# Performance work log

Hardware: AMD Instinct MI355X
Metric: run time of the kernel (lower is better)

Reference implementation:

```python
import jax, jax.numpy as jnp
import numpy as np

ALPHA = 0.65   # module default
KSIZE = 7      # kernel_size
T = 1.0        # forward arg t default


def setup_inputs() -> dict:
    key = jax.random.key(0)
    k1, k2 = jax.random.split(key)
    x = jax.random.normal(k1, (4, 32, 128, 128), dtype=jnp.float32)
    dil_metric = jax.random.normal(k2, (32, 2, 2), dtype=jnp.float32)
    return {"x": x, "dil_metric": dil_metric}


def _kernel(dil_metric):
    # y grid: [k,k,2] integer offsets centered at floor(k/2) (matches get_y)
    c = jnp.arange(KSIZE, dtype=jnp.float32) - (KSIZE // 2)
    yi, yj = jnp.meshgrid(c, c, indexing="ij")
    y = jnp.stack([yi, yj], axis=-1)                       # [k,k,2]
    Dy = jnp.einsum("cab,ijb->cija", dil_metric, y)        # [C,k,k,2]
    sumsq = jnp.sum(Dy * Dy, axis=-1)                      # [C,k,k] = norm^2
    p = 2.0 * ALPHA / (2.0 * ALPHA - 1.0)
    const = T * (2.0 * ALPHA - 1.0) / (2.0 * ALPHA * T) ** p
    # const * norm**p written as const * (norm^2)^(p/2) (same math, smooth at 0)
    return const * jnp.power(sumsq, p / 2.0)               # [C,k,k]


def reference(x, dil_metric):
    # dilation: -inf_convolution_2d(-x, kernel)
    kern = _kernel(dil_metric)                             # [C,k,k]
    H, W = x.shape[2], x.shape[3]
    pad = (KSIZE - 1) // 2                                 # k odd -> symmetric pad
    xp = jnp.pad(-x, ((0, 0), (0, 0), (pad, pad), (pad, pad)))  # zero pad like torch
    out = None
    # fixed small k*k loop over window offsets; min-plus conv without im2col blowup
    for i in range(KSIZE):
        for j in range(KSIZE):
            v = xp[:, :, i:i + H, j:j + W] + kern[:, i, j][None, :, None, None]
            out = v if out is None else jnp.minimum(out, v)
    return -out
```

## Files before the change

kernel.cpp:

```cpp
#include <hip/hip_runtime.h>
#include <math.h>

#define KS   7
#define PAD  3
#define TH   8
#define W128 128
#define HALO_H (TH + KS - 1)
#define HALO_W (W128 + KS - 1)

__global__ __launch_bounds__(256) void dilation_r2_kernel(
    const float* __restrict__ x,
    const float* __restrict__ dm,
    float* __restrict__ out)
{
    __shared__ float ksm[KS * KS];
    __shared__ float sx[HALO_H][HALO_W];

    const int tid  = threadIdx.x;
    const int tile = blockIdx.x;
    const int c    = blockIdx.y;
    const int n    = blockIdx.z;
    const int h0   = tile * TH;

    if (tid < KS * KS) {
        const int i = tid / KS, j = tid % KS;
        const float yi = (float)(i - PAD);
        const float yj = (float)(j - PAD);
        const float m00 = dm[c * 4 + 0], m01 = dm[c * 4 + 1];
        const float m10 = dm[c * 4 + 2], m11 = dm[c * 4 + 3];
        const float d0 = m00 * yi + m01 * yj;
        const float d1 = m10 * yi + m11 * yj;
        const float s  = d0 * d0 + d1 * d1;
        const float pc = (float)(0.3 / pow(1.3, 13.0 / 3.0));
        ksm[tid] = pc * powf(s, (float)(13.0 / 6.0));
    }

    const float* xc = x + ((size_t)(n * 32 + c)) * (W128 * W128);
    for (int idx = tid; idx < HALO_H * HALO_W; idx += 256) {
        const int r  = idx / HALO_W;
        const int cc = idx - r * HALO_W;
        const int gh = h0 + r - PAD;
        const int gw = cc - PAD;
        float v = 0.0f;
        if (gh >= 0 && gh < W128 && gw >= 0 && gw < W128)
            v = xc[gh * W128 + gw];
        sx[r][cc] = v;
    }
    __syncthreads();

    const int w  = tid & (W128 - 1);
    const int hq = (tid >> 7) * 4;
    float acc0 = -INFINITY, acc1 = -INFINITY, acc2 = -INFINITY, acc3 = -INFINITY;

    #pragma unroll
    for (int j = 0; j < KS; ++j) {
        float col[TH / 2 + KS - 1];
        #pragma unroll
        for (int r = 0; r < TH / 2 + KS - 1; ++r)
            col[r] = sx[hq + r][w + j];
        #pragma unroll
        for (int i = 0; i < KS; ++i) {
            const float k = ksm[i * KS + j];
            acc0 = fmaxf(acc0, col[i + 0] - k);
            acc1 = fmaxf(acc1, col[i + 1] - k);
            acc2 = fmaxf(acc2, col[i + 2] - k);
            acc3 = fmaxf(acc3, col[i + 3] - k);
        }
    }

    float* oc = out + ((size_t)(n * 32 + c)) * (W128 * W128) + (h0 + hq) * W128 + w;
    oc[0 * W128] = acc0;
    oc[1 * W128] = acc1;
    oc[2 * W128] = acc2;
    oc[3 * W128] = acc3;
}

extern "C" void kernel_launch(void* const* d_in, const int* in_sizes, int n_in,
                              void* d_out, int out_size, void* d_ws, size_t ws_size,
                              hipStream_t stream) {
    const float* x  = (const float*)d_in[0];
    const float* dm = (const float*)d_in[1];
    float* out = (float*)d_out;

    dim3 grid(W128 / TH, 32, 4);
    dim3 block(256);
    dilation_r2_kernel<<<grid, block, 0, stream>>>(x, dm, out);
}
```

Measured before the change: 13.41 us.

## Use taller tiles with 4x4 register blocking and vectorized loads/stores

Tile height grows from 8 to 32 rows, so the halo overhead per block shrinks, and the grid drops from 2048 blocks to 512. Global loads and stores now use float4, and shared memory rows are padded to a stride of 136. Each thread computes a 4x4 output patch from rows held in registers, with the negated kernel kept in registers and pre-folded into the min-plus taps. The risks are fewer blocks to hide latency on a large GPU and higher register pressure.

```diff
diff --git a/kernel.cpp b/kernel.cpp
--- a/kernel.cpp
+++ b/kernel.cpp
@@ -1,78 +1,112 @@
 #include <hip/hip_runtime.h>
 #include <math.h>
 
-#define KS   7
-#define PAD  3
-#define TH   8
-#define W128 128
-#define HALO_H (TH + KS - 1)
-#define HALO_W (W128 + KS - 1)
+typedef float f4 __attribute__((ext_vector_type(4)));
 
-__global__ __launch_bounds__(256) void dilation_r2_kernel(
+#define KS     7
+#define W      128
+#define TILE_H 32
+#define HALO_H (TILE_H + KS - 1)
+#define STR    136
+#define CHK    (STR / 4)
+#define NCHK   (HALO_H * CHK)
+
+__global__ __launch_bounds__(256) void dil_kernel(
     const float* __restrict__ x,
     const float* __restrict__ dm,
     float* __restrict__ out)
 {
-    __shared__ float ksm[KS * KS];
-    __shared__ float sx[HALO_H][HALO_W];
+    __shared__ __align__(16) float ksm[52];
+    __shared__ __align__(16) float sx[HALO_H * STR];
 
-    const int tid  = threadIdx.x;
-    const int tile = blockIdx.x;
-    const int c    = blockIdx.y;
-    const int n    = blockIdx.z;
-    const int h0   = tile * TH;
+    const int tid = threadIdx.x;
+    const int c   = blockIdx.y;
+    const int n   = blockIdx.z;
+    const int h0  = blockIdx.x * TILE_H;
 
-    if (tid < KS * KS) {
-        const int i = tid / KS, j = tid % KS;
-        const float yi = (float)(i - PAD);
-        const float yj = (float)(j - PAD);
-        const float m00 = dm[c * 4 + 0], m01 = dm[c * 4 + 1];
-        const float m10 = dm[c * 4 + 2], m11 = dm[c * 4 + 3];
-        const float d0 = m00 * yi + m01 * yj;
-        const float d1 = m10 * yi + m11 * yj;
-        const float s  = d0 * d0 + d1 * d1;
-        const float pc = (float)(0.3 / pow(1.3, 13.0 / 3.0));
-        ksm[tid] = pc * powf(s, (float)(13.0 / 6.0));
+    if (tid < 52) {
+        float v = -1e30f;
+        if (tid < 49) {
+            const int i = tid / KS, j = tid % KS;
+            const float yi = (float)(i - 3), yj = (float)(j - 3);
+            const float m00 = dm[c*4+0], m01 = dm[c*4+1];
+            const float m10 = dm[c*4+2], m11 = dm[c*4+3];
+            const float d0 = m00*yi + m01*yj;
+            const float d1 = m10*yi + m11*yj;
+            const float s  = d0*d0 + d1*d1;
+            const float pc = (float)(0.3 / pow(1.3, 13.0/3.0));
+            v = -(pc * powf(s, (float)(13.0/6.0)));
+        }
+        ksm[tid] = v;
     }
 
-    const float* xc = x + ((size_t)(n * 32 + c)) * (W128 * W128);
-    for (int idx = tid; idx < HALO_H * HALO_W; idx += 256) {
-        const int r  = idx / HALO_W;
-        const int cc = idx - r * HALO_W;
-        const int gh = h0 + r - PAD;
-        const int gw = cc - PAD;
-        float v = 0.0f;
-        if (gh >= 0 && gh < W128 && gw >= 0 && gw < W128)
-            v = xc[gh * W128 + gw];
-        sx[r][cc] = v;
+    const float* xc = x + ((size_t)(n*32 + c)) * (W*W);
+    #pragma unroll
+    for (int it = 0; it < 6; ++it) {
+        const int idx = tid + it*256;
+        if (idx < NCHK) {
+            const int r  = idx / CHK;
+            const int m  = idx - r*CHK;
+            const int gh = h0 + r - 3;
+            f4 v = {0.f, 0.f, 0.f, 0.f};
+            if (m >= 1 && m <= 32 && gh >= 0 && gh < W)
+                v = *reinterpret_cast<const f4*>(xc + gh*W + (m-1)*4);
+            *reinterpret_cast<f4*>(sx + idx*4) = v;
+        }
     }
     __syncthreads();
 
-    const int w  = tid & (W128 - 1);
-    const int hq = (tid >> 7) * 4;
-    float acc0 = -INFINITY, acc1 = -INFINITY, acc2 = -INFINITY, acc3 = -INFINITY;
+    f4 kr[13];
+    #pragma unroll
+    for (int q = 0; q < 13; ++q)
+        kr[q] = *reinterpret_cast<const f4*>(ksm + q*4);
+#define NK(i, j) kr[((i)*KS + (j)) >> 2][((i)*KS + (j)) & 3]
+
+    const int w4 = (tid & 31) * 4;
+    const int hr = (tid >> 5) * 4;
+
+    float acc[4][4];
+    #pragma unroll
+    for (int o = 0; o < 4; ++o)
+        #pragma unroll
+        for (int q = 0; q < 4; ++q)
+            acc[o][q] = -INFINITY;
 
     #pragma unroll
-    for (int j = 0; j < KS; ++j) {
-        float col[TH / 2 + KS - 1];
+    for (int r = 0; r < 10; ++r) {
+        const float* row = sx + (hr + r) * STR + w4;
+        const f4 a0 = *reinterpret_cast<const f4*>(row);
+        const f4 a1 = *reinterpret_cast<const f4*>(row + 4);
+        const f4 a2 = *reinterpret_cast<const f4*>(row + 8);
+        float rw[12] = {a0[0],a0[1],a0[2],a0[3],
+                        a1[0],a1[1],a1[2],a1[3],
+                        a2[0],a2[1],a2[2],a2[3]};
         #pragma unroll
-        for (int r = 0; r < TH / 2 + KS - 1; ++r)
-            col[r] = sx[hq + r][w + j];
-        #pragma unroll
-        for (int i = 0; i < KS; ++i) {
-            const float k = ksm[i * KS + j];
-            acc0 = fmaxf(acc0, col[i + 0] - k);
-            acc1 = fmaxf(acc1, col[i + 1] - k);
-            acc2 = fmaxf(acc2, col[i + 2] - k);
-            acc3 = fmaxf(acc3, col[i + 3] - k);
+        for (int o = 0; o < 4; ++o) {
+            const int i = r - o;
+            if (i < 0 || i >= KS) continue;
+            #pragma unroll
+            for (int q = 0; q < 4; ++q) {
+                const float t0 = rw[q+1] + NK(i,0);
+                const float t1 = rw[q+2] + NK(i,1);
+                const float t2 = rw[q+3] + NK(i,2);
+                const float t3 = rw[q+4] + NK(i,3);
+                const float t4 = rw[q+5] + NK(i,4);
+                const float t5 = rw[q+6] + NK(i,5);
+                const float t6 = rw[q+7] + NK(i,6);
+                const float m1 = fmaxf(fmaxf(t0, t1), t2);
+                const float m2 = fmaxf(fmaxf(t3, t4), t5);
+                acc[o][q] = fmaxf(fmaxf(m1, m2), fmaxf(t6, acc[o][q]));
+            }
         }
     }
 
-    float* oc = out + ((size_t)(n * 32 + c)) * (W128 * W128) + (h0 + hq) * W128 + w;
-    oc[0 * W128] = acc0;
-    oc[1 * W128] = acc1;
-    oc[2 * W128] = acc2;
-    oc[3 * W128] = acc3;
+    float* oc = out + ((size_t)(n*32 + c)) * (W*W) + (h0 + hr) * W + w4;
+    #pragma unroll
+    for (int o = 0; o < 4; ++o) {
+        f4 v = {acc[o][0], acc[o][1], acc[o][2], acc[o][3]};
+        *reinterpret_cast<f4*>(oc + o*W) = v;
+    }
 }
 
 extern "C" void kernel_launch(void* const* d_in, const int* in_sizes, int n_in,
@@ -82,7 +116,7 @@
     const float* dm = (const float*)d_in[1];
     float* out = (float*)d_out;
 
-    dim3 grid(W128 / TH, 32, 4);
+    dim3 grid(W / TILE_H, 32, 4);
     dim3 block(256);
-    dilation_r2_kernel<<<grid, block, 0, stream>>>(x, dm, out);
+    dil_kernel<<<grid, block, 0, stream>>>(x, dm, out);
 }
```

After: 12.06 us. 1.11x faster.
